# Kernel optimization log

Measured on AMD Instinct MI355X. Metric: run time of the kernel, lower is better.

## Reference

```python
import jax, jax.numpy as jnp
import numpy as np

B, IN, H, O, T = 4096, 128, 1024, 64, 25  # batch, static feat, hidden, outputs, steps


def setup_inputs() -> dict:
    key = jax.random.key(0)
    ks = jax.random.split(key, 11)
    s = 1.0 / np.sqrt(H)  # PyTorch LSTM/Linear uniform init scale
    u = lambda k, sh: jax.random.uniform(k, sh, jnp.float32, -s, s)
    return {
        "static_input": jax.random.normal(ks[0], (B, IN), jnp.float32),
        "W_ih0": u(ks[1], (4 * H, IN + O)),
        "W_hh0": u(ks[2], (4 * H, H)),
        "b_ih0": u(ks[3], (4 * H,)),
        "b_hh0": u(ks[4], (4 * H,)),
        "W_ih1": u(ks[5], (4 * H, H)),
        "W_hh1": u(ks[6], (4 * H, H)),
        "b_ih1": u(ks[7], (4 * H,)),
        "b_hh1": u(ks[8], (4 * H,)),
        "W_out": u(ks[9], (O, H)),
        "b_out": u(ks[10], (O,)),
        "num_steps": T,
    }


def _lstm_cell(x, h, c, W_ih, W_hh, b):
    # PyTorch gate order: input, forget, cell(g), output
    g = x @ W_ih.T + h @ W_hh.T + b
    i, f, gg, o = jnp.split(g, 4, axis=-1)
    c_new = jax.nn.sigmoid(f) * c + jax.nn.sigmoid(i) * jnp.tanh(gg)
    h_new = jax.nn.sigmoid(o) * jnp.tanh(c_new)
    return h_new, c_new


def reference(static_input, W_ih0, W_hh0, b_ih0, b_hh0,
              W_ih1, W_hh1, b_ih1, b_hh1, W_out, b_out, num_steps):
    b0 = b_ih0 + b_hh0
    b1 = b_ih1 + b_hh1
    batch = static_input.shape[0]
    hid = W_hh0.shape[1]
    out_dim = W_out.shape[0]
    z = jnp.zeros((batch, hid), jnp.float32)
    y0 = jnp.zeros((batch, out_dim), jnp.float32)  # output_seq[:, 0] is zeros at t=0

    def step(carry, _):
        h1, c1, h2, c2, y_prev = carry
        x = jnp.concatenate([static_input, y_prev], axis=-1)  # [B, IN+O]
        h1, c1 = _lstm_cell(x, h1, c1, W_ih0, W_hh0, b0)
        h2, c2 = _lstm_cell(h1, h2, c2, W_ih1, W_hh1, b1)
        y = h2 @ W_out.T + b_out  # [B, O]
        return (h1, c1, h2, c2, y), y

    _, ys = jax.lax.scan(step, (z, z, z, z, y0), None, length=num_steps)
    return jnp.transpose(ys, (1, 0, 2))  # [B, T, O]
```

## Files before the change

kernel.cpp:

```cpp
#include <hip/hip_runtime.h>

#define BATCH  4096
#define HID    1024
#define NOUT   64
#define TSTEPS 25
#define KA2    1280
#define KA2R   1216
#define KB     2048
#define LDY    1600

typedef __attribute__((ext_vector_type(8))) __bf16 bf16x8;
typedef __attribute__((ext_vector_type(4))) float  floatx4;

__device__ __forceinline__ unsigned short f2bf(float f) {
    union { float f; unsigned u; } v; v.f = f;
    unsigned r = v.u + 0x7fffu + ((v.u >> 16) & 1u);
    return (unsigned short)(r >> 16);
}
__device__ __forceinline__ float rcpf(float x) { return __builtin_amdgcn_rcpf(x); }
__device__ __forceinline__ float sigmf(float x) { return rcpf(1.0f + __expf(-x)); }
__device__ __forceinline__ float tanh_fast(float x) {
    float ax = fabsf(x);
    float e  = __expf(-2.0f * ax);
    float t  = (1.0f - e) * rcpf(1.0f + e);
    return copysignf(t, x);
}

#define GLDS16(gp, lp) __builtin_amdgcn_global_load_lds( \
    (const __attribute__((address_space(1))) void*)(gp), \
    (__attribute__((address_space(3))) void*)(lp), 16, 0, 0)

__global__ __launch_bounds__(512, 2) void lstm_gate_gemm(
    const unsigned short* __restrict__ X, int K,
    const unsigned short* __restrict__ W,
    const float* __restrict__ ginit,
    float* __restrict__ cell,
    unsigned short* __restrict__ d1, int ld1, int off1,
    unsigned short* __restrict__ d2, int ld2, int off2,
    float* __restrict__ dfp)
{
    __shared__ __align__(16) char smem[131072];

    const int tid  = threadIdx.x;
    const int lane = tid & 63;
    const int w    = tid >> 6;
    const int ql   = lane >> 4;
    const int lr   = lane & 15;
    const int wr   = w >> 2;
    const int wc   = w & 3;

    const int id  = blockIdx.y * 16 + blockIdx.x;
    const int xcd = id & 7;
    const int c   = id >> 3;
    const int bx  = (xcd & 3) * 4 + (c & 3);
    const int by  = (xcd >> 2) * 8 + (c >> 2);
    const int m0  = bx * 256;
    const int j0  = by * 64;

    const int s0  = w * 128 + lane;
    const int r0  = s0 >> 3;
    const int kc0 = (s0 & 7) ^ (r0 & 7);
    const unsigned sOff = (unsigned)s0 * 16;
    const unsigned short* sA[2];
    const unsigned short* sB[2];
    sA[0] = X + (size_t)(m0 + r0) * K + kc0 * 8;
    sA[1] = X + (size_t)(m0 + 128 + r0) * K + kc0 * 8;
    {
        const int nb0 = r0, nb1 = 128 + r0;
        sB[0] = W + (size_t)((nb0 & 3) * HID + j0 + (nb0 >> 2)) * K + kc0 * 8;
        sB[1] = W + (size_t)((nb1 & 3) * HID + j0 + (nb1 >> 2)) * K + kc0 * 8;
    }

#define STAGE_A(h, tt, p) do { \
    const unsigned short* _s = sA[h] + (size_t)(tt) * 64; \
    char* _d = smem + (p) * 65536 + (h) * 16384 + sOff; \
    GLDS16(_s, _d); \
    GLDS16(_s + 8 * (size_t)K, _d + 1024); \
} while (0)

#define STAGE_B(h, tt, p) do { \
    const unsigned short* _s = sB[h] + (size_t)(tt) * 64; \
    char* _d = smem + (p) * 65536 + 32768 + (h) * 16384 + sOff; \
    GLDS16(_s, _d); \
    GLDS16(_s + 2 * (size_t)K, _d + 1024); \
} while (0)

    unsigned offA[4], offB[2];
#pragma unroll
    for (int fi = 0; fi < 4; ++fi) {
        int r = wr * 64 + fi * 16 + lr;
        offA[fi] = (unsigned)((r * 8 + (ql ^ (r & 7))) * 16);
    }
#pragma unroll
    for (int fj = 0; fj < 2; ++fj) {
        int r = wc * 32 + fj * 16 + lr;
        offB[fj] = (unsigned)(32768 + (r * 8 + (ql ^ (r & 7))) * 16);
    }

    floatx4 acc[4][4][2];
#pragma unroll
    for (int q = 0; q < 4; ++q)
#pragma unroll
        for (int i = 0; i < 4; ++i)
#pragma unroll
            for (int j = 0; j < 2; ++j)
                acc[q][i][j] = floatx4{0.f, 0.f, 0.f, 0.f};

    const int NT = K >> 6;

    STAGE_A(0, 0, 0); STAGE_B(0, 0, 0); STAGE_A(1, 0, 0); STAGE_B(1, 0, 0);
    STAGE_B(0, 1, 1); STAGE_A(1, 1, 1);
    asm volatile("s_waitcnt vmcnt(4)");
    __builtin_amdgcn_s_barrier();

#define LOAD_A(AV, HALF) do { \
    const char* _ab = smem + cur + (HALF) * 16384; \
    _Pragma("unroll") \
    for (int fi = 0; fi < 4; ++fi) { \
        AV[fi][0] = *(const bf16x8*)(_ab + offA[fi]); \
        AV[fi][1] = *(const bf16x8*)(_ab + (offA[fi] ^ 64u)); \
    } \
} while (0)

#define LOAD_B(BV, HALF) do { \
    const char* _bb = smem + cur + (HALF) * 16384; \
    _Pragma("unroll") \
    for (int fj = 0; fj < 2; ++fj) { \
        BV[fj][0] = *(const bf16x8*)(_bb + offB[fj]); \
        BV[fj][1] = *(const bf16x8*)(_bb + (offB[fj] ^ 64u)); \
    } \
} while (0)

#define MFMA_PHASE(Q, AV, BV) do { \
    __builtin_amdgcn_s_barrier(); \
    asm volatile("s_waitcnt lgkmcnt(0)"); \
    __builtin_amdgcn_sched_barrier(0); \
    __builtin_amdgcn_s_setprio(1); \
    _Pragma("unroll") \
    for (int fi = 0; fi < 4; ++fi) \
    _Pragma("unroll") \
    for (int fj = 0; fj < 2; ++fj) \
    _Pragma("unroll") \
    for (int kk = 0; kk < 2; ++kk) \
        acc[Q][fi][fj] = __builtin_amdgcn_mfma_f32_16x16x32_bf16( \
            AV[fi][kk], BV[fj][kk], acc[Q][fi][fj], 0, 0, 0); \
    __builtin_amdgcn_s_setprio(0); \
    __builtin_amdgcn_s_barrier(); \
} while (0)

    int par = 0;
    for (int t = 0; t < NT; ++t) {
        const int cur = par * 65536;
        const int np  = par ^ 1;
        const int t1  = (t + 1 < NT) ? t + 1 : NT - 1;
        const int t2  = (t + 2 < NT) ? t + 2 : NT - 1;
        bf16x8 av[4][2], bv0[2][2], bv1[2][2];
        LOAD_A(av, 0); LOAD_B(bv0, 0);
        STAGE_A(0, t1, np);
        MFMA_PHASE(0, av, bv0);
        LOAD_B(bv1, 1);
        STAGE_B(1, t1, np);
        MFMA_PHASE(1, av, bv1);
        LOAD_A(av, 1);
        STAGE_B(0, t2, par);
        MFMA_PHASE(2, av, bv1);
        STAGE_A(1, t2, par);
        asm volatile("s_waitcnt vmcnt(4)");
        MFMA_PHASE(3, av, bv0);
        par ^= 1;
    }

    asm volatile("s_waitcnt vmcnt(0)");
    __builtin_amdgcn_s_barrier();

    float* scratch = (float*)(void*)smem + w * 640;
    const int jj   = lane & 7;
    const int rsel = lane >> 3;

#pragma unroll
    for (int qd = 0; qd < 4; ++qd) {
        const int qa = (qd >= 2) ? 1 : 0;
        const int qb = (qd == 1 || qd == 2) ? 1 : 0;
        const int rowbase = m0 + qa * 128 + wr * 64;
        const int jg = j0 + qb * 32 + wc * 8 + jj;
        const float4 gi = *(const float4*)(ginit + (size_t)jg * 4);
#pragma unroll
        for (int fi = 0; fi < 4; ++fi) {
#pragma unroll
            for (int fj = 0; fj < 2; ++fj)
#pragma unroll
                for (int r = 0; r < 4; ++r)
                    scratch[(ql * 4 + r) * 36 + fj * 16 + lr] = acc[qd][fi][fj][r];
            asm volatile("" ::: "memory");
#pragma unroll
            for (int p = 0; p < 2; ++p) {
                const int row = rsel + p * 8;
                const float4 g = *(const float4*)(scratch + row * 36 + jj * 4);
                const int b = rowbase + fi * 16 + row;
                float iv = sigmf(g.x + gi.x);
                float fv = sigmf(g.y + gi.y);
                float gv = tanh_fast(g.z + gi.z);
                float ov = sigmf(g.w + gi.w);
                size_t ci = (size_t)b * HID + jg;
                float cn = fv * cell[ci] + iv * gv;
                cell[ci] = cn;
                float hv = ov * tanh_fast(cn);
                unsigned short hb = f2bf(hv);
                d1[(size_t)b * ld1 + off1 + jg] = hb;
                if (d2)  d2[(size_t)b * ld2 + off2 + jg] = hb;
                if (dfp) dfp[(size_t)b * HID + jg] = hv;
            }
            asm volatile("" ::: "memory");
        }
    }
#undef MFMA_PHASE
#undef LOAD_A
#undef LOAD_B
#undef STAGE_A
#undef STAGE_B
}

__global__ __launch_bounds__(256) void out_gemm(
    const float* __restrict__ h2, const float* __restrict__ wt,
    const float* __restrict__ bout, float* __restrict__ y,
    unsigned short* __restrict__ xn)
{
    __shared__ float hl[8 * 1024];
    const int tid = threadIdx.x;
    const int b0 = blockIdx.x * 8;
#pragma unroll
    for (int r = 0; r < 8; ++r) {
        int f4 = r * 256 + tid;
        *(float4*)(hl + f4 * 4) = *(const float4*)(h2 + (size_t)b0 * 1024 + f4 * 4);
    }
    __syncthreads();
    const int o  = tid & 63;
    const int wv = tid >> 6;
    float acc0 = 0.f, acc1 = 0.f;
#pragma unroll 8
    for (int k = 0; k < 1024; ++k) {
        float wvv = wt[k * 64 + o];
        acc0 += hl[(wv * 2 + 0) * 1024 + k] * wvv;
        acc1 += hl[(wv * 2 + 1) * 1024 + k] * wvv;
    }
    float bo = bout[o];
    int b = b0 + wv * 2;
    float y0 = acc0 + bo, y1 = acc1 + bo;
    y[(size_t)b * LDY + o] = y0;
    y[(size_t)(b + 1) * LDY + o] = y1;
    xn[(size_t)b * KA2 + o] = f2bf(y0);
    xn[(size_t)(b + 1) * KA2 + o] = f2bf(y1);
}

__global__ void build_woutT(const float* __restrict__ wout, float* __restrict__ wt)
{
    int idx = blockIdx.x * 256 + threadIdx.x;
    int o = idx & 63, k = idx >> 6;
    wt[idx] = wout[(size_t)o * 1024 + k];
}

__global__ void build_bias(const float* __restrict__ a, const float* __restrict__ b,
                           float* __restrict__ o)
{
    int idx = blockIdx.x * 256 + threadIdx.x;
    int gate = idx & 3, j = idx >> 2;
    int n = gate * 1024 + j;
    o[idx] = a[n] + b[n];
}

__global__ __launch_bounds__(256) void build_w0(
    const float* __restrict__ wih, const float* __restrict__ whh,
    unsigned short* __restrict__ w0)
{
    int idx = blockIdx.x * 256 + threadIdx.x;
    int n = idx / 320;
    int c = (idx - n * 320) * 4;
    float4 v = {0.f, 0.f, 0.f, 0.f};
    if (c < 64)        v = *(const float4*)(wih + (size_t)n * 192 + 128 + c);
    else if (c < 192)  v = *(const float4*)(wih + (size_t)n * 192 + (c - 64));
    else if (c < 1216) v = *(const float4*)(whh + (size_t)n * 1024 + (c - 192));
    ushort4 o;
    o.x = f2bf(v.x); o.y = f2bf(v.y); o.z = f2bf(v.z); o.w = f2bf(v.w);
    *(ushort4*)(w0 + (size_t)n * KA2 + c) = o;
}

__global__ __launch_bounds__(256) void build_w1(
    const float* __restrict__ wih, const float* __restrict__ whh,
    unsigned short* __restrict__ w1)
{
    int idx = blockIdx.x * 256 + threadIdx.x;
    int n = idx >> 9;
    int c = (idx & 511) * 4;
    float4 v;
    if (c < 1024) v = *(const float4*)(wih + (size_t)n * 1024 + c);
    else          v = *(const float4*)(whh + (size_t)n * 1024 + (c - 1024));
    ushort4 o;
    o.x = f2bf(v.x); o.y = f2bf(v.y); o.z = f2bf(v.z); o.w = f2bf(v.w);
    *(ushort4*)(w1 + (size_t)n * KB + c) = o;
}

__global__ __launch_bounds__(256) void build_x0static(
    const float* __restrict__ stat, unsigned short* __restrict__ xa,
    unsigned short* __restrict__ xb)
{
    int idx = blockIdx.x * 256 + threadIdx.x;
    int b = idx >> 5;
    int c = (idx & 31) * 4;
    float4 v = *(const float4*)(stat + (size_t)b * 128 + c);
    ushort4 o;
    o.x = f2bf(v.x); o.y = f2bf(v.y); o.z = f2bf(v.z); o.w = f2bf(v.w);
    *(ushort4*)(xa + (size_t)b * KA2 + 64 + c) = o;
    *(ushort4*)(xb + (size_t)b * KA2 + 64 + c) = o;
}

extern "C" void kernel_launch(void* const* d_in, const int* in_sizes, int n_in,
                              void* d_out, int out_size, void* d_ws, size_t ws_size,
                              hipStream_t stream)
{
    (void)in_sizes; (void)n_in; (void)out_size; (void)ws_size;
    const float* static_in = (const float*)d_in[0];
    const float* Wih0 = (const float*)d_in[1];
    const float* Whh0 = (const float*)d_in[2];
    const float* bih0 = (const float*)d_in[3];
    const float* bhh0 = (const float*)d_in[4];
    const float* Wih1 = (const float*)d_in[5];
    const float* Whh1 = (const float*)d_in[6];
    const float* bih1 = (const float*)d_in[7];
    const float* bhh1 = (const float*)d_in[8];
    const float* Wout = (const float*)d_in[9];
    const float* bout = (const float*)d_in[10];
    float* out = (float*)d_out;

    char* p = (char*)d_ws;
    size_t off = 0;
    auto take = [&](size_t n) { char* r = p + off; off += (n + 255) & ~(size_t)255; return r; };

    unsigned short* W0   = (unsigned short*)take((size_t)4096 * KA2 * 2);
    unsigned short* W1   = (unsigned short*)take((size_t)4096 * KB * 2);
    float*          B1b  = (float*)take(4096 * 4);
    float*          B0b  = (float*)take(4096 * 4);
    float*          WoT  = (float*)take((size_t)1024 * 64 * 4);
    float*          H2f  = (float*)take((size_t)BATCH * HID * 4);
    float*          C1   = (float*)take((size_t)BATCH * HID * 4);
    float*          C2   = (float*)take((size_t)BATCH * HID * 4);
    unsigned short* X0a  = (unsigned short*)take((size_t)BATCH * KA2 * 2);
    unsigned short* X0b  = (unsigned short*)take((size_t)BATCH * KA2 * 2);
    unsigned short* X1a  = (unsigned short*)take((size_t)BATCH * KB * 2);
    unsigned short* X1b  = (unsigned short*)take((size_t)BATCH * KB * 2);

    hipMemsetAsync(C1, 0, (size_t)BATCH * HID * 4, stream);
    hipMemsetAsync(C2, 0, (size_t)BATCH * HID * 4, stream);
    hipMemsetAsync(X0a, 0, (size_t)BATCH * KA2 * 2, stream);
    hipMemsetAsync(X0b, 0, (size_t)BATCH * KA2 * 2, stream);
    hipMemsetAsync(X1a, 0, (size_t)BATCH * KB * 2, stream);

    build_w0<<<5120, 256, 0, stream>>>(Wih0, Whh0, W0);
    build_w1<<<8192, 256, 0, stream>>>(Wih1, Whh1, W1);
    build_woutT<<<256, 256, 0, stream>>>(Wout, WoT);
    build_bias<<<16, 256, 0, stream>>>(bih0, bhh0, B0b);
    build_bias<<<16, 256, 0, stream>>>(bih1, bhh1, B1b);
    build_x0static<<<512, 256, 0, stream>>>(static_in, X0a, X0b);

    dim3 grid(16, 16);
    for (int t = 0; t < TSTEPS; ++t) {
        unsigned short* X0c = (t & 1) ? X0b : X0a;
        unsigned short* X0n = (t & 1) ? X0a : X0b;
        unsigned short* X1c = (t & 1) ? X1b : X1a;
        unsigned short* X1n = (t & 1) ? X1a : X1b;
        lstm_gate_gemm<<<grid, 512, 0, stream>>>(X0c, KA2, W0, B0b, C1,
                                                 X1c, KB, 0, X0n, KA2, 192, nullptr);
        lstm_gate_gemm<<<grid, 512, 0, stream>>>(X1c, KB, W1, B1b, C2,
                                                 X1n, KB, 1024, nullptr, 0, 0, H2f);
        out_gemm<<<512, 256, 0, stream>>>(H2f, WoT, bout, out + t * NOUT, X0n);
    }
}
```

Baseline: 3.973 ms.

## Software-pipeline LDS fragment loads with MFMA phases using double register sets

New measurement: 3.939 ms. No clear change (-0.8%).

```diff
diff --git a/kernel.cpp b/kernel.cpp
--- a/kernel.cpp
+++ b/kernel.cpp
@@ -73,14 +73,14 @@
 
 #define STAGE_A(h, tt, p) do { \
     const unsigned short* _s = sA[h] + (size_t)(tt) * 64; \
-    char* _d = smem + (p) * 65536 + (h) * 16384 + sOff; \
+    char* _d = smem + (p) + (h) * 16384 + sOff; \
     GLDS16(_s, _d); \
     GLDS16(_s + 8 * (size_t)K, _d + 1024); \
 } while (0)
 
 #define STAGE_B(h, tt, p) do { \
     const unsigned short* _s = sB[h] + (size_t)(tt) * 64; \
-    char* _d = smem + (p) * 65536 + 32768 + (h) * 16384 + sOff; \
+    char* _d = smem + (p) + 32768 + (h) * 16384 + sOff; \
     GLDS16(_s, _d); \
     GLDS16(_s + 2 * (size_t)K, _d + 1024); \
 } while (0)
@@ -97,24 +97,8 @@
         offB[fj] = (unsigned)(32768 + (r * 8 + (ql ^ (r & 7))) * 16);
     }
 
-    floatx4 acc[4][4][2];
-#pragma unroll
-    for (int q = 0; q < 4; ++q)
-#pragma unroll
-        for (int i = 0; i < 4; ++i)
-#pragma unroll
-            for (int j = 0; j < 2; ++j)
-                acc[q][i][j] = floatx4{0.f, 0.f, 0.f, 0.f};
-
-    const int NT = K >> 6;
-
-    STAGE_A(0, 0, 0); STAGE_B(0, 0, 0); STAGE_A(1, 0, 0); STAGE_B(1, 0, 0);
-    STAGE_B(0, 1, 1); STAGE_A(1, 1, 1);
-    asm volatile("s_waitcnt vmcnt(4)");
-    __builtin_amdgcn_s_barrier();
-
-#define LOAD_A(AV, HALF) do { \
-    const char* _ab = smem + cur + (HALF) * 16384; \
+#define LOAD_A(AV, BASE) do { \
+    const char* _ab = smem + (BASE); \
     _Pragma("unroll") \
     for (int fi = 0; fi < 4; ++fi) { \
         AV[fi][0] = *(const bf16x8*)(_ab + offA[fi]); \
@@ -122,8 +106,8 @@
     } \
 } while (0)
 
-#define LOAD_B(BV, HALF) do { \
-    const char* _bb = smem + cur + (HALF) * 16384; \
+#define LOAD_B(BV, BASE) do { \
+    const char* _bb = smem + (BASE); \
     _Pragma("unroll") \
     for (int fj = 0; fj < 2; ++fj) { \
         BV[fj][0] = *(const bf16x8*)(_bb + offB[fj]); \
@@ -131,10 +115,7 @@
     } \
 } while (0)
 
-#define MFMA_PHASE(Q, AV, BV) do { \
-    __builtin_amdgcn_s_barrier(); \
-    asm volatile("s_waitcnt lgkmcnt(0)"); \
-    __builtin_amdgcn_sched_barrier(0); \
+#define MFMA16(Q, AV, BV) do { \
     __builtin_amdgcn_s_setprio(1); \
     _Pragma("unroll") \
     for (int fi = 0; fi < 4; ++fi) \
@@ -145,28 +126,64 @@
         acc[Q][fi][fj] = __builtin_amdgcn_mfma_f32_16x16x32_bf16( \
             AV[fi][kk], BV[fj][kk], acc[Q][fi][fj], 0, 0, 0); \
     __builtin_amdgcn_s_setprio(0); \
-    __builtin_amdgcn_s_barrier(); \
-} while (0)
+} while (0)
+
+    floatx4 acc[4][4][2];
+#pragma unroll
+    for (int q = 0; q < 4; ++q)
+#pragma unroll
+        for (int i = 0; i < 4; ++i)
+#pragma unroll
+            for (int j = 0; j < 2; ++j)
+                acc[q][i][j] = floatx4{0.f, 0.f, 0.f, 0.f};
+
+    const int NT = K >> 6;
+
+    bf16x8 av0[4][2], av1[4][2], bv0[2][2], bv1[2][2];
+
+    STAGE_A(0, 0, 0); STAGE_B(0, 0, 0); STAGE_A(1, 0, 0); STAGE_B(1, 0, 0);
+    STAGE_B(0, 1, 65536); STAGE_A(1, 1, 65536);
+    asm volatile("s_waitcnt vmcnt(4)");
+    __builtin_amdgcn_s_barrier();
+    __builtin_amdgcn_sched_barrier(0);
+    LOAD_A(av0, 0);
+    LOAD_B(bv0, 0);
+    LOAD_B(bv1, 16384);
+    __builtin_amdgcn_sched_barrier(0);
 
     int par = 0;
     for (int t = 0; t < NT; ++t) {
-        const int cur = par * 65536;
-        const int np  = par ^ 1;
+        const int cur = par << 16;
+        const int np  = cur ^ 65536;
         const int t1  = (t + 1 < NT) ? t + 1 : NT - 1;
         const int t2  = (t + 2 < NT) ? t + 2 : NT - 1;
-        bf16x8 av[4][2], bv0[2][2], bv1[2][2];
-        LOAD_A(av, 0); LOAD_B(bv0, 0);
+        __builtin_amdgcn_s_barrier();
+        __builtin_amdgcn_sched_barrier(0);
+        LOAD_A(av1, cur + 16384);
         STAGE_A(0, t1, np);
-        MFMA_PHASE(0, av, bv0);
-        LOAD_B(bv1, 1);
+        __builtin_amdgcn_sched_barrier(0);
+        MFMA16(0, av0, bv0);
+        __builtin_amdgcn_s_barrier();
+        __builtin_amdgcn_sched_barrier(0);
         STAGE_B(1, t1, np);
-        MFMA_PHASE(1, av, bv1);
-        LOAD_A(av, 1);
-        STAGE_B(0, t2, par);
-        MFMA_PHASE(2, av, bv1);
-        STAGE_A(1, t2, par);
-        asm volatile("s_waitcnt vmcnt(4)");
-        MFMA_PHASE(3, av, bv0);
+        __builtin_amdgcn_sched_barrier(0);
+        MFMA16(1, av0, bv1);
+        asm volatile("s_waitcnt vmcnt(2)");
+        __builtin_amdgcn_s_barrier();
+        __builtin_amdgcn_sched_barrier(0);
+        LOAD_A(av0, np);
+        STAGE_B(0, t2, cur);
+        __builtin_amdgcn_sched_barrier(0);
+        MFMA16(2, av1, bv1);
+        asm volatile("s_waitcnt vmcnt(2)");
+        __builtin_amdgcn_s_barrier();
+        __builtin_amdgcn_sched_barrier(0);
+        LOAD_B(bv1, np + 16384);
+        STAGE_A(1, t2, cur);
+        __builtin_amdgcn_sched_barrier(0);
+        MFMA16(3, av1, bv0);
+        __builtin_amdgcn_sched_barrier(0);
+        LOAD_B(bv0, np);
         par ^= 1;
     }
 
@@ -213,7 +230,7 @@
             asm volatile("" ::: "memory");
         }
     }
-#undef MFMA_PHASE
+#undef MFMA16
 #undef LOAD_A
 #undef LOAD_B
 #undef STAGE_A
```
